# Kernel optimization log

Measured on AMD Instinct MI355X. Metric: run time of the kernel, lower is better.

## Reference

```python
import jax, jax.numpy as jnp
import numpy as np

VOCAB = 50257
EMBED = 128
BATCH = 4096
CTX = 8


def setup_inputs() -> dict:
    key = jax.random.key(0)
    k_idx, k_proj, k_pred = jax.random.split(key, 3)
    initrange = 1.0 / np.sqrt(EMBED)
    inp = jax.random.randint(k_idx, (BATCH, CTX), 0, VOCAB, dtype=jnp.int64)
    W_proj = jax.random.uniform(k_proj, (VOCAB, EMBED), dtype=jnp.float32,
                                minval=-initrange, maxval=initrange)
    W_pred = jax.random.uniform(k_pred, (EMBED, VOCAB), dtype=jnp.float32,
                                minval=-initrange, maxval=initrange)
    return {"input": inp, "W_proj": W_proj, "W_pred": W_pred}


def reference(input, W_proj, W_pred):
    # Original builds a [1, V] count (one-hot sum) vector then does count @ W_proj.
    # That is mathematically identical to gathering embedding rows for each
    # context index and summing (duplicates accumulate), which is the efficient
    # embedding-bag form. Batched over B contexts.
    ctx_emb = jnp.take(W_proj, input, axis=0)      # [B, C, E] gather
    word_emb = jnp.sum(ctx_emb, axis=1)            # [B, E] bag-sum
    word_pred_logit = word_emb @ W_pred            # [B, V] vocab logits
    return word_pred_logit
```

## Files before the change

kernel.cpp:

```cpp
#include <hip/hip_runtime.h>
#include <hip/hip_bf16.h>

#define VOCAB 50257
#define EMBED 128
#define BATCH 4096
#define CTX   8

#define BM 128
#define NXT 786
#define VPAD 50304
#define LDSP 136

#define CHUNKS 50
#define NBAND 64
#define NTICK (NBAND * CHUNKS)

typedef __attribute__((ext_vector_type(8))) short bf16x8;
typedef __attribute__((ext_vector_type(4))) float f32x4;
typedef float f32x4u __attribute__((ext_vector_type(4), aligned(4)));

static __device__ __forceinline__ ushort f2bf(float f) {
  __hip_bfloat16 h = __float2bfloat16(f);
  return *reinterpret_cast<ushort*>(&h);
}

__global__ __launch_bounds__(256) void embed_bag_kernel(
    const int* __restrict__ idx, const float* __restrict__ Wp,
    __hip_bfloat16* __restrict__ emb) {
  int wave = threadIdx.x >> 6;
  int lane = threadIdx.x & 63;
  int row  = blockIdx.x * 4 + wave;
  const int* ri = idx + row * CTX;
  int e0 = lane * 2;
  float s0 = 0.f, s1 = 0.f;
#pragma unroll
  for (int c = 0; c < CTX; ++c) {
    int w = ri[c];
    float2 wv = *reinterpret_cast<const float2*>(Wp + (size_t)w * EMBED + e0);
    s0 += wv.x; s1 += wv.y;
  }
  __hip_bfloat162 pv;
  pv.x = __float2bfloat16(s0);
  pv.y = __float2bfloat16(s1);
  *reinterpret_cast<__hip_bfloat162*>(emb + (size_t)row * EMBED + e0) = pv;
}

__global__ __launch_bounds__(256) void transpose_b_kernel(
    const float* __restrict__ Bm, ushort* __restrict__ Btf) {
  __shared__ ushort Bs[64 * LDSP];
  int x = blockIdx.x;
  int cbase = x * 64;
  int tid = threadIdx.x;
  bool edge = (cbase + 64 > VOCAB);
#pragma unroll
  for (int i = 0; i < 8; ++i) {
    int c  = tid + i * 256;
    int e  = c >> 4;
    int v4 = (c & 15) << 2;
    int col = cbase + v4;
    float4 b;
    if (!edge) {
      b = *reinterpret_cast<const float4*>(Bm + (size_t)e * VOCAB + col);
    } else {
      b.x = (col + 0 < VOCAB) ? Bm[(size_t)e * VOCAB + col + 0] : 0.f;
      b.y = (col + 1 < VOCAB) ? Bm[(size_t)e * VOCAB + col + 1] : 0.f;
      b.z = (col + 2 < VOCAB) ? Bm[(size_t)e * VOCAB + col + 2] : 0.f;
      b.w = (col + 3 < VOCAB) ? Bm[(size_t)e * VOCAB + col + 3] : 0.f;
    }
    Bs[(v4 + 0) * LDSP + e] = f2bf(b.x);
    Bs[(v4 + 1) * LDSP + e] = f2bf(b.y);
    Bs[(v4 + 2) * LDSP + e] = f2bf(b.z);
    Bs[(v4 + 3) * LDSP + e] = f2bf(b.w);
  }
  __syncthreads();
  int lane = tid & 63, wv = tid >> 6;
  int lr = lane & 15, lg = lane >> 4;
#pragma unroll
  for (int p = 0; p < 4; ++p) {
    int instr = p * 4 + wv;
    int kq = instr >> 2, n = instr & 3;
    int v  = n * 16 + lr;
    int e0 = kq * 32 + lg * 8;
    uint4 val = *reinterpret_cast<const uint4*>(&Bs[v * LDSP + e0]);
    *reinterpret_cast<uint4*>(Btf + (size_t)x * 8192 + instr * 512 + lane * 8) = val;
  }
}

__global__ __launch_bounds__(256, 2) void gemm11_kernel(
    const ushort* __restrict__ A,
    const ushort* __restrict__ Btf,
    float* __restrict__ C,
    unsigned int* __restrict__ cnt) {
  __shared__ float Cs[4][64 * 68];
  __shared__ unsigned int sT;

  int tid  = threadIdx.x;
  int lane = tid & 63;
  int wv   = tid >> 6;
  int lr   = lane & 15;
  int lg   = lane >> 4;

  float* Csw = &Cs[wv][0];
  int wbase = lane * 68;
  int rbas  = (lane & 3) * 16;
  int nofs  = (lane >> 2) * 4;

  for (;;) {
    __syncthreads();
    if (tid == 0) sT = atomicAdd(cnt, 1u);
    __syncthreads();
    unsigned int t = sT;
    if (t >= NTICK) break;

    int band = (int)(t / CHUNKS);
    int c    = (int)(t % CHUNKS);
    int R0   = band * 64 + wv * 16;

    const ushort* Ag = A + (size_t)R0 * EMBED;
    bf16x8 af[4];
#pragma unroll
    for (int kq = 0; kq < 4; ++kq)
      af[kq] = *reinterpret_cast<const bf16x8*>(
          Ag + lr * EMBED + kq * 32 + lg * 8);

    int ngr = (c < CHUNKS - 1) ? 4 : 1;
    for (int gg = 0; gg < ngr; ++gg) {
      int g = c * 4 + gg;
      const ushort* Bg0 = Btf + (size_t)(g * 4) * 8192 + lane * 8;
      if (g != 196) {
#pragma unroll
        for (int ni = 0; ni < 16; ++ni) {
          const ushort* Bp = Bg0 + (size_t)(ni >> 2) * 8192;
          int n = ni & 3;
          bf16x8 b[4];
#pragma unroll
          for (int kq = 0; kq < 4; ++kq)
            b[kq] = *reinterpret_cast<const bf16x8*>(Bp + (kq * 4 + n) * 512);
          f32x4 acc = {0.f, 0.f, 0.f, 0.f};
#pragma unroll
          for (int kq = 0; kq < 4; ++kq)
            acc = __builtin_amdgcn_mfma_f32_16x16x32_bf16(b[kq], af[kq], acc, 0, 0, 0);
          *reinterpret_cast<f32x4*>(&Csw[wbase + ni * 4]) = acc;
        }
        f32x4 v[16];
#pragma unroll
        for (int r = 0; r < 16; ++r)
          v[r] = *reinterpret_cast<const f32x4*>(&Csw[(rbas + r) * 68 + nofs]);
        int colbase = g * 256 + lane * 4;
#pragma unroll
        for (int r = 0; r < 16; ++r)
          *reinterpret_cast<f32x4u*>(C + (size_t)(R0 + r) * VOCAB + colbase) =
              __builtin_bit_cast(f32x4u, v[r]);
      } else {
#pragma unroll
        for (int ni = 0; ni < 8; ++ni) {
          const ushort* Bp = Bg0 + (size_t)(ni >> 2) * 8192;
          int n = ni & 3;
          bf16x8 b[4];
#pragma unroll
          for (int kq = 0; kq < 4; ++kq)
            b[kq] = *reinterpret_cast<const bf16x8*>(Bp + (kq * 4 + n) * 512);
          f32x4 acc = {0.f, 0.f, 0.f, 0.f};
#pragma unroll
          for (int kq = 0; kq < 4; ++kq)
            acc = __builtin_amdgcn_mfma_f32_16x16x32_bf16(b[kq], af[kq], acc, 0, 0, 0);
          *reinterpret_cast<f32x4*>(&Csw[wbase + ni * 4]) = acc;
        }
        int colbase = 196 * 256 + lane * 4;
#pragma unroll
        for (int r = 0; r < 16; ++r) {
          if (lane < 21) {
            f32x4 v = *reinterpret_cast<const f32x4*>(&Csw[(rbas + r) * 68 + nofs]);
            float* cp = C + (size_t)(R0 + r) * VOCAB + colbase;
            if (lane < 20) {
              *reinterpret_cast<f32x4u*>(cp) = __builtin_bit_cast(f32x4u, v);
            } else {
              cp[0] = v[0];
            }
          }
        }
      }
    }
  }
}

#define FLDSP 132
__global__ __launch_bounds__(256, 4) void gemm_kernel(
    const __hip_bfloat16* __restrict__ A,
    const float* __restrict__ Bm,
    float* __restrict__ C) {
  __shared__ char BsRaw[64 * FLDSP * 2];
  int bid = blockIdx.x;
  int k8  = bid & 7;
  int j   = bid >> 3;
  int t   = j >> 5;
  int y   = j & 31;
  int x   = k8 + t * 8;
  if (x >= NXT) return;

  int tid  = threadIdx.x;
  int lane = tid & 63;
  int wv   = tid >> 6;
  int lr   = lane & 15;
  int lg   = lane >> 4;
  int r0   = wv * 32;

  const ushort* Ag = reinterpret_cast<const ushort*>(A) + (size_t)(y * BM) * EMBED;
  uint4 a_raw[2][4];
#pragma unroll
  for (int m = 0; m < 2; ++m)
#pragma unroll
    for (int kq = 0; kq < 4; ++kq)
      a_raw[m][kq] = *reinterpret_cast<const uint4*>(
          Ag + (r0 + m * 16 + lr) * EMBED + kq * 32 + lg * 8);

  int cbase = x * 64;
  bool edge = (x == NXT - 1);
  float4 bb[8];
#pragma unroll
  for (int i = 0; i < 8; ++i) {
    int c  = tid + i * 256;
    int e  = c >> 4;
    int v4 = (c & 15) << 2;
    int col = cbase + v4;
    if (!edge) {
      bb[i] = *reinterpret_cast<const float4*>(Bm + (size_t)e * VOCAB + col);
    } else {
      bb[i].x = (col + 0 < VOCAB) ? Bm[(size_t)e * VOCAB + col + 0] : 0.f;
      bb[i].y = (col + 1 < VOCAB) ? Bm[(size_t)e * VOCAB + col + 1] : 0.f;
      bb[i].z = (col + 2 < VOCAB) ? Bm[(size_t)e * VOCAB + col + 2] : 0.f;
      bb[i].w = (col + 3 < VOCAB) ? Bm[(size_t)e * VOCAB + col + 3] : 0.f;
    }
  }
#pragma unroll
  for (int i = 0; i < 8; ++i) {
    int c  = tid + i * 256;
    int e  = c >> 4;
    int v4 = (c & 15) << 2;
    float vals[4] = {bb[i].x, bb[i].y, bb[i].z, bb[i].w};
#pragma unroll
    for (int jj = 0; jj < 4; ++jj) {
      int v   = v4 + jj;
      int off = v * (FLDSP * 2) + ((e * 2) ^ ((v & 28) << 2));
      *reinterpret_cast<ushort*>(BsRaw + off) = f2bf(vals[jj]);
    }
  }
  __syncthreads();

  f32x4 acc[2][4] = {};
#pragma unroll
  for (int kq = 0; kq < 4; ++kq) {
    int ebyte = (kq * 32 + lg * 8) * 2;
    bf16x8 bfr[4];
#pragma unroll
    for (int n = 0; n < 4; ++n) {
      int v   = n * 16 + lr;
      int off = v * (FLDSP * 2) + (ebyte ^ ((v & 28) << 2));
      bfr[n] = *reinterpret_cast<const bf16x8*>(BsRaw + off);
    }
#pragma unroll
    for (int m = 0; m < 2; ++m) {
      bf16x8 af = __builtin_bit_cast(bf16x8, a_raw[m][kq]);
#pragma unroll
      for (int n = 0; n < 4; ++n)
        acc[m][n] = __builtin_amdgcn_mfma_f32_16x16x32_bf16(af, bfr[n], acc[m][n], 0, 0, 0);
    }
  }

  size_t crow0 = (size_t)y * BM + r0;
#pragma unroll
  for (int m = 0; m < 2; ++m) {
#pragma unroll
    for (int n = 0; n < 4; ++n) {
      int colc = cbase + n * 16 + lr;
      if (colc < VOCAB) {
        float* cp = C + (crow0 + m * 16 + lg * 4) * (size_t)VOCAB + colc;
#pragma unroll
        for (int q = 0; q < 4; ++q)
          cp[(size_t)q * VOCAB] = acc[m][n][q];
      }
    }
  }
}

extern "C" void kernel_launch(void* const* d_in, const int* in_sizes, int n_in,
                              void* d_out, int out_size, void* d_ws, size_t ws_size,
                              hipStream_t stream) {
  const int*   idx    = (const int*)d_in[0];
  const float* W_proj = (const float*)d_in[1];
  const float* W_pred = (const float*)d_in[2];
  float*       out    = (float*)d_out;

  __hip_bfloat16* emb = (__hip_bfloat16*)d_ws;
  ushort* Btf = (ushort*)((char*)d_ws + (size_t)1048576);
  unsigned int* cnt = (unsigned int*)((char*)d_ws + (size_t)14680064);
  const size_t needed = (size_t)14680064 + 64;

  embed_bag_kernel<<<BATCH / 4, 256, 0, stream>>>(idx, W_proj, emb);

  if (ws_size >= needed) {
    transpose_b_kernel<<<NXT, 256, 0, stream>>>(W_pred, Btf);
    hipMemsetAsync(cnt, 0, sizeof(unsigned int), stream);
    gemm11_kernel<<<512, 256, 0, stream>>>((const ushort*)emb, Btf, out, cnt);
  } else {
    int strips = (NXT + 7) / 8;
    int grid = 8 * strips * 32;
    gemm_kernel<<<grid, 256, 0, stream>>>(emb, W_pred, out);
  }
}
```

Before: 372.8 us.

## Halve per-group column width to cut LDS and double occupancy in gemm

The persistent GEMM kernel now processes 128-column groups instead of 256. This halves the per-wave LDS staging buffer and allows 4 blocks per CU with a 1024-block grid. The LDS-to-global store remap is rewritten so each half-wave writes a different row with 128 contiguous floats, and the chunk count is adjusted to cover the same columns. The aim is more waves in flight to hide memory latency on the output-write-bound GEMM, at the cost of more atomic tick fetches and fewer registers per thread.

```diff
diff --git a/kernel.cpp b/kernel.cpp
--- a/kernel.cpp
+++ b/kernel.cpp
@@ -11,7 +11,7 @@
 #define VPAD 50304
 #define LDSP 136
 
-#define CHUNKS 50
+#define CHUNKS 99
 #define NBAND 64
 #define NTICK (NBAND * CHUNKS)
 
@@ -86,12 +86,12 @@
   }
 }
 
-__global__ __launch_bounds__(256, 2) void gemm11_kernel(
+__global__ __launch_bounds__(256, 4) void gemm12_kernel(
     const ushort* __restrict__ A,
     const ushort* __restrict__ Btf,
     float* __restrict__ C,
     unsigned int* __restrict__ cnt) {
-  __shared__ float Cs[4][64 * 68];
+  __shared__ float Cs[4][64 * 36];
   __shared__ unsigned int sT;
 
   int tid  = threadIdx.x;
@@ -101,9 +101,11 @@
   int lg   = lane >> 4;
 
   float* Csw = &Cs[wv][0];
-  int wbase = lane * 68;
-  int rbas  = (lane & 3) * 16;
-  int nofs  = (lane >> 2) * 4;
+  int wbase = lane * 36;
+  int row_off = lane >> 5;
+  int c4   = lane & 31;
+  int rni  = c4 >> 2;
+  int rlg  = c4 & 3;
 
   for (;;) {
     __syncthreads();
@@ -126,10 +128,10 @@
     int ngr = (c < CHUNKS - 1) ? 4 : 1;
     for (int gg = 0; gg < ngr; ++gg) {
       int g = c * 4 + gg;
-      const ushort* Bg0 = Btf + (size_t)(g * 4) * 8192 + lane * 8;
-      if (g != 196) {
-#pragma unroll
-        for (int ni = 0; ni < 16; ++ni) {
+      const ushort* Bg0 = Btf + (size_t)(g * 2) * 8192 + lane * 8;
+      if (g != 392) {
+#pragma unroll
+        for (int ni = 0; ni < 8; ++ni) {
           const ushort* Bp = Bg0 + (size_t)(ni >> 2) * 8192;
           int n = ni & 3;
           bf16x8 b[4];
@@ -142,15 +144,18 @@
             acc = __builtin_amdgcn_mfma_f32_16x16x32_bf16(b[kq], af[kq], acc, 0, 0, 0);
           *reinterpret_cast<f32x4*>(&Csw[wbase + ni * 4]) = acc;
         }
-        f32x4 v[16];
-#pragma unroll
-        for (int r = 0; r < 16; ++r)
-          v[r] = *reinterpret_cast<const f32x4*>(&Csw[(rbas + r) * 68 + nofs]);
-        int colbase = g * 256 + lane * 4;
-#pragma unroll
-        for (int r = 0; r < 16; ++r)
-          *reinterpret_cast<f32x4u*>(C + (size_t)(R0 + r) * VOCAB + colbase) =
-              __builtin_bit_cast(f32x4u, v[r]);
+        f32x4 v[8];
+#pragma unroll
+        for (int p = 0; p < 8; ++p) {
+          int srcl = rlg * 16 + p * 2 + row_off;
+          v[p] = *reinterpret_cast<const f32x4*>(&Csw[srcl * 36 + rni * 4]);
+        }
+        int colbase = g * 128 + c4 * 4;
+#pragma unroll
+        for (int p = 0; p < 8; ++p)
+          *reinterpret_cast<f32x4u*>(
+              C + (size_t)(R0 + p * 2 + row_off) * VOCAB + colbase) =
+              __builtin_bit_cast(f32x4u, v[p]);
       } else {
 #pragma unroll
         for (int ni = 0; ni < 8; ++ni) {
@@ -166,13 +171,14 @@
             acc = __builtin_amdgcn_mfma_f32_16x16x32_bf16(b[kq], af[kq], acc, 0, 0, 0);
           *reinterpret_cast<f32x4*>(&Csw[wbase + ni * 4]) = acc;
         }
-        int colbase = 196 * 256 + lane * 4;
-#pragma unroll
-        for (int r = 0; r < 16; ++r) {
-          if (lane < 21) {
-            f32x4 v = *reinterpret_cast<const f32x4*>(&Csw[(rbas + r) * 68 + nofs]);
-            float* cp = C + (size_t)(R0 + r) * VOCAB + colbase;
-            if (lane < 20) {
+        int colbase = 392 * 128 + c4 * 4;
+#pragma unroll
+        for (int p = 0; p < 8; ++p) {
+          if (c4 < 21) {
+            int srcl = rlg * 16 + p * 2 + row_off;
+            f32x4 v = *reinterpret_cast<const f32x4*>(&Csw[srcl * 36 + rni * 4]);
+            float* cp = C + (size_t)(R0 + p * 2 + row_off) * VOCAB + colbase;
+            if (c4 < 20) {
               *reinterpret_cast<f32x4u*>(cp) = __builtin_bit_cast(f32x4u, v);
             } else {
               cp[0] = v[0];
@@ -301,7 +307,7 @@
   if (ws_size >= needed) {
     transpose_b_kernel<<<NXT, 256, 0, stream>>>(W_pred, Btf);
     hipMemsetAsync(cnt, 0, sizeof(unsigned int), stream);
-    gemm11_kernel<<<512, 256, 0, stream>>>((const ushort*)emb, Btf, out, cnt);
+    gemm12_kernel<<<1024, 256, 0, stream>>>((const ushort*)emb, Btf, out, cnt);
   } else {
     int strips = (NXT + 7) / 8;
     int grid = 8 * strips * 32;
```

Result: slower. 392.6 us (+5.3%).
